# Kernel optimization log

Measured on AMD Instinct MI355X. Metric: run time of the kernel, lower is better.

Reference implementation:

```python
import jax, jax.numpy as jnp
import numpy as np

HS, FF, NH = 1024, 4096, 16
HD = HS // NH
EPS = 1e-5

def _ln(x, g, b):
    m = jnp.mean(x, axis=-1, keepdims=True)
    v = jnp.mean((x - m) ** 2, axis=-1, keepdims=True)
    return (x - m) * jax.lax.rsqrt(v + EPS) * g + b

def setup_inputs() -> dict:
    key = jax.random.key(0)
    ks = jax.random.split(key, 12)
    s = 1.0 / np.sqrt(HS)
    si = 1.0 / np.sqrt(FF)
    d = {
        "hidden_states": jax.random.normal(ks[0], (2, 2048, HS), dtype=jnp.float32),
        "attention_mask": jnp.zeros((2, 1, 1, 2048), dtype=jnp.float32),
        "Wq": jax.random.uniform(ks[1], (HS, HS), minval=-s, maxval=s),
        "bq": jnp.zeros((HS,), jnp.float32),
        "Wk": jax.random.uniform(ks[2], (HS, HS), minval=-s, maxval=s),
        "bk": jnp.zeros((HS,), jnp.float32),
        "Wv": jax.random.uniform(ks[3], (HS, HS), minval=-s, maxval=s),
        "bv": jnp.zeros((HS,), jnp.float32),
        "Wo": jax.random.uniform(ks[4], (HS, HS), minval=-s, maxval=s),
        "bo": jnp.zeros((HS,), jnp.float32),
        "W1": jax.random.uniform(ks[5], (HS, FF), minval=-s, maxval=s),
        "b1": jnp.zeros((FF,), jnp.float32),
        "W2": jax.random.uniform(ks[6], (FF, HS), minval=-si, maxval=si),
        "b2": jnp.zeros((HS,), jnp.float32),
        "ln1_g": jnp.ones((HS,), jnp.float32),
        "ln1_b": jnp.zeros((HS,), jnp.float32),
        "ln2_g": jnp.ones((HS,), jnp.float32),
        "ln2_b": jnp.zeros((HS,), jnp.float32),
    }
    return d

def reference(hidden_states, attention_mask, Wq, bq, Wk, bk, Wv, bv, Wo, bo,
              W1, b1, W2, b2, ln1_g, ln1_b, ln2_g, ln2_b):
    bs, S, _ = hidden_states.shape
    x = hidden_states
    # self-attention (dropout is identity in eval)
    q = (x @ Wq + bq).reshape(bs, S, NH, HD).transpose(0, 2, 1, 3)
    k = (x @ Wk + bk).reshape(bs, S, NH, HD).transpose(0, 2, 1, 3)
    v = (x @ Wv + bv).reshape(bs, S, NH, HD).transpose(0, 2, 1, 3)
    scores = jnp.einsum("bhqd,bhkd->bhqk", q, k) / np.sqrt(HD) + attention_mask
    probs = jax.nn.softmax(scores, axis=-1)
    attn = jnp.einsum("bhqk,bhkd->bhqd", probs, v)
    attn = attn.transpose(0, 2, 1, 3).reshape(bs, S, HS)
    mha = attn @ Wo + bo
    h = _ln(x + mha, ln1_g, ln1_b)
    # FFN
    ff = jax.nn.relu(h @ W1 + b1) @ W2 + b2
    return _ln(h + ff, ln2_g, ln2_b)
```

## Files before the change

kernel.cpp:

```cpp
#include <hip/hip_runtime.h>
#include <hip/hip_bf16.h>

#define HS   1024
#define FF   4096
#define NH   16
#define HD   64
#define SEQ  2048
#define BSZ  2
#define MROWS (BSZ * SEQ)
#define EPS  1e-5f
#define QKV_STRIDE (3 * HS)

typedef float f32x4  __attribute__((ext_vector_type(4)));
typedef short bf16x8 __attribute__((ext_vector_type(8)));

#if __has_builtin(__builtin_amdgcn_exp2f)
#define EXP2(x) __builtin_amdgcn_exp2f(x)
#else
#define EXP2(x) exp2f(x)
#endif

__device__ __forceinline__ unsigned short f2bf(float x) {
  unsigned int u = __float_as_uint(x);
  u += 0x7fffu + ((u >> 16) & 1u);
  return (unsigned short)(u >> 16);
}

__device__ __forceinline__ float bf2f(unsigned short u) {
  return __uint_as_float((unsigned int)u << 16);
}

__device__ __forceinline__ unsigned int pkbf(float a, float b) {
  union { __hip_bfloat162 h; unsigned int u; } x;
  x.h = __float22bfloat162_rn(float2{a, b});
  return x.u;
}

__device__ __forceinline__ void async16(const ushort* g, ushort* lds) {
  __builtin_amdgcn_global_load_lds(
      (const __attribute__((address_space(1))) unsigned int*)g,
      (__attribute__((address_space(3))) unsigned int*)lds, 16, 0, 0);
}

template <int TBM, int TBN, bool RELU, bool OUT_BF16, bool PARTIAL>
__global__ __launch_bounds__(256) void gemm_bf16_kernel(
    const ushort* __restrict__ A, const ushort* __restrict__ Bt,
    const float* __restrict__ bias, void* __restrict__ Cout,
    int M, int N, int K, int kLen, size_t zstride)
{
  constexpr int MI = TBM / 32;
  constexpr int NJ = TBN / 32;
  __shared__ ushort As[TBM * 64];
  __shared__ ushort Bs[TBN * 64];

  const int tid = threadIdx.x;
  const int wv = tid >> 6, ln = tid & 63;

  const unsigned nxy = gridDim.x * gridDim.y;
  unsigned id = blockIdx.y * gridDim.x + blockIdx.x;
  id = (id & 7) * (nxy >> 3) + (id >> 3);
  const int bn = id % gridDim.x, bm = id / gridDim.x;

  const int lr = ln & 15;
  const int lg = ln >> 4;
  const int mrow_base = (wv >> 1) * (TBM / 2);
  const int ncol_base = (wv & 1) * (TBN / 2);

  f32x4 acc[MI][NJ];
#pragma unroll
  for (int i = 0; i < MI; ++i)
#pragma unroll
    for (int j = 0; j < NJ; ++j) acc[i][j] = (f32x4){0.f, 0.f, 0.f, 0.f};

  const int rr = ln >> 3, cc = ln & 7;
  const int kBeg = blockIdx.z * kLen, kEnd = kBeg + kLen;

  for (int k0 = kBeg; k0 < kEnd; k0 += 64) {
    __syncthreads();
#pragma unroll
    for (int t = 0; t < TBM / 32; ++t) {
      const int R = wv * (TBM / 4) + t * 8 + rr;
      const int c = cc ^ (R & 7);
      async16(A + (size_t)(bm * TBM + R) * K + k0 + c * 8,
              &As[(size_t)(wv * (TBM / 4) + t * 8) * 64]);
    }
#pragma unroll
    for (int t = 0; t < TBN / 32; ++t) {
      const int R = wv * (TBN / 4) + t * 8 + rr;
      const int c = cc ^ (R & 7);
      async16(Bt + (size_t)(bn * TBN + R) * K + k0 + c * 8,
              &Bs[(size_t)(wv * (TBN / 4) + t * 8) * 64]);
    }
    __syncthreads();

#pragma unroll
    for (int s = 0; s < 2; ++s) {
      bf16x8 a[MI], b[NJ];
#pragma unroll
      for (int i = 0; i < MI; ++i) {
        const int m = mrow_base + i * 16 + lr;
        a[i] = *(const bf16x8*)&As[(size_t)m * 64 + (((s * 4 + lg) ^ (m & 7)) * 8)];
      }
#pragma unroll
      for (int j = 0; j < NJ; ++j) {
        const int n = ncol_base + j * 16 + lr;
        b[j] = *(const bf16x8*)&Bs[(size_t)n * 64 + (((s * 4 + lg) ^ (n & 7)) * 8)];
      }
#pragma unroll
      for (int i = 0; i < MI; ++i)
#pragma unroll
        for (int j = 0; j < NJ; ++j)
          acc[i][j] = __builtin_amdgcn_mfma_f32_16x16x32_bf16(a[i], b[j], acc[i][j], 0, 0, 0);
    }
  }

  const int gm0 = bm * TBM + mrow_base;
  const int gn0 = bn * TBN + ncol_base;

  if (PARTIAL) {
    float* Cp = (float*)Cout + (size_t)blockIdx.z * zstride;
#pragma unroll
    for (int i = 0; i < MI; ++i)
#pragma unroll
      for (int r = 0; r < 4; ++r) {
        const size_t row = (size_t)(gm0 + i * 16 + lg * 4 + r);
#pragma unroll
        for (int j = 0; j < NJ; ++j)
          Cp[row * N + gn0 + j * 16 + lr] = acc[i][j][r];
      }
  } else {
    float bs4[NJ];
#pragma unroll
    for (int j = 0; j < NJ; ++j) bs4[j] = bias[gn0 + j * 16 + lr];
    float* Cf = (float*)Cout;
    ushort* Cb = (ushort*)Cout;
#pragma unroll
    for (int i = 0; i < MI; ++i) {
#pragma unroll
      for (int r = 0; r < 4; ++r) {
        const size_t row = (size_t)(gm0 + i * 16 + lg * 4 + r);
#pragma unroll
        for (int j = 0; j < NJ; ++j) {
          float val = acc[i][j][r] + bs4[j];
          if (RELU) val = fmaxf(val, 0.f);
          const size_t idx = row * N + gn0 + j * 16 + lr;
          if (OUT_BF16) Cb[idx] = f2bf(val);
          else          Cf[idx] = val;
        }
      }
    }
  }
}

__device__ __forceinline__ void transpose_tile(
    const float* __restrict__ W, ushort* __restrict__ Wt,
    int K, int N, int n0, int k0, int tid, ushort (*T)[72])
{
#pragma unroll
  for (int t = 0; t < 4; ++t) {
    const int r = t * 16 + (tid >> 4);
    const int c = (tid & 15) * 4;
    const float4 w = *(const float4*)&W[(size_t)(k0 + r) * N + n0 + c];
    T[c + 0][r] = f2bf(w.x); T[c + 1][r] = f2bf(w.y);
    T[c + 2][r] = f2bf(w.z); T[c + 3][r] = f2bf(w.w);
  }
  __syncthreads();
#pragma unroll
  for (int t = 0; t < 4; ++t) {
    const int n = t * 16 + (tid >> 4);
    const int kc = (tid & 15) * 4;
    ushort4 o;
    o.x = T[n][kc]; o.y = T[n][kc + 1]; o.z = T[n][kc + 2]; o.w = T[n][kc + 3];
    *(ushort4*)&Wt[(size_t)(n0 + n) * K + k0 + kc] = o;
  }
}

__global__ __launch_bounds__(256) void prep_kernel(
    const float* __restrict__ Wq, const float* __restrict__ Wk,
    const float* __restrict__ Wv, const float* __restrict__ Wo,
    const float* __restrict__ W1, const float* __restrict__ W2,
    const float* __restrict__ bq, const float* __restrict__ bk,
    const float* __restrict__ bv, const float* __restrict__ x,
    const float* __restrict__ mask,
    ushort* __restrict__ Wqkvt, ushort* __restrict__ Wot,
    ushort* __restrict__ W1t, ushort* __restrict__ W2t,
    float* __restrict__ bqkv, ushort* __restrict__ xb,
    float* __restrict__ maskL2)
{
  __shared__ ushort T[64][72];
  const int b = blockIdx.x, tid = threadIdx.x;
  const size_t M1 = 1024 * 1024;
  if (b < 1024) {
    const int w = b >> 8, l = b & 255;
    const int n0 = (l & 15) * 64, k0 = (l >> 4) * 64;
    const float* src = (w == 0) ? Wq : (w == 1) ? Wk : (w == 2) ? Wv : Wo;
    ushort* dst = (w < 3) ? (Wqkvt + (size_t)w * M1) : Wot;
    transpose_tile(src, dst, HS, HS, n0, k0, tid, T);
  } else if (b < 2048) {
    const int l = b - 1024;
    transpose_tile(W1, W1t, HS, FF, (l & 63) * 64, (l >> 6) * 64, tid, T);
  } else if (b < 3072) {
    const int l = b - 2048;
    transpose_tile(W2, W2t, FF, HS, (l & 15) * 64, (l >> 4) * 64, tid, T);
  } else if (b < 5120) {
    const size_t base = (size_t)(b - 3072) * 2048 + tid * 8;
    const float4 v0 = *(const float4*)&x[base];
    const float4 v1 = *(const float4*)&x[base + 4];
    ushort4 o0, o1;
    o0.x = f2bf(v0.x); o0.y = f2bf(v0.y); o0.z = f2bf(v0.z); o0.w = f2bf(v0.w);
    o1.x = f2bf(v1.x); o1.y = f2bf(v1.y); o1.z = f2bf(v1.z); o1.w = f2bf(v1.w);
    *(ushort4*)&xb[base] = o0;
    *(ushort4*)&xb[base + 4] = o1;
  } else {
#pragma unroll
    for (int t = 0; t < 12; ++t) {
      const int i = t * 256 + tid;
      bqkv[i] = (i < HS) ? bq[i] : (i < 2 * HS) ? bk[i - HS] : bv[i - 2 * HS];
    }
#pragma unroll
    for (int t = 0; t < 16; ++t) {
      const int i = t * 256 + tid;
      maskL2[i] = mask[i] * 1.44269504f;
    }
  }
}

__global__ __launch_bounds__(256) void vtrans_kernel(
    const ushort* __restrict__ vb, ushort* __restrict__ VTg, int stride)
{
  __shared__ ushort T[64][68];
  const int tid = threadIdx.x;
  const int s0 = blockIdx.x * 64;
  const int bh = blockIdx.y;
  const int b = bh >> 4, h = bh & 15;
#pragma unroll
  for (int t = 0; t < 4; ++t) {
    const int rr = t * 16 + (tid >> 4);
    const int c4 = (tid & 15) * 4;
    const ushort4 w = *(const ushort4*)&vb[(size_t)(b * SEQ + s0 + rr) * stride + h * 64 + c4];
    T[c4 + 0][rr] = w.x; T[c4 + 1][rr] = w.y;
    T[c4 + 2][rr] = w.z; T[c4 + 3][rr] = w.w;
  }
  __syncthreads();
#pragma unroll
  for (int t = 0; t < 4; ++t) {
    const int d = t * 16 + (tid >> 4);
    const int k4 = (tid & 15) * 4;
    ushort4 o;
    o.x = T[d][k4]; o.y = T[d][k4 + 1]; o.z = T[d][k4 + 2]; o.w = T[d][k4 + 3];
    *(ushort4*)&VTg[((size_t)bh * 64 + d) * SEQ + s0 + k4] = o;
  }
}

__global__ __launch_bounds__(256, 2) void attention_mfma_kernel(
    const ushort* __restrict__ Qb, const ushort* __restrict__ Kb,
    const ushort* __restrict__ VTg, const float* __restrict__ maskL2,
    ushort* __restrict__ O)
{
  __shared__ ushort smem[36864];
  float* mL = (float*)(smem + 32768);

  const int tid = threadIdx.x;
  const int wv = tid >> 6, ln = tid & 63;
  const int c = ln & 15, g = ln >> 4;

  const unsigned d0 = blockIdx.x + 16u * (blockIdx.y + 16u * blockIdx.z);
  const unsigned w0 = (d0 & 7) * 64 + (d0 >> 3);
  const int qt = w0 & 15;
  const int hh = (w0 >> 4) & 15;
  const int b  = w0 >> 8;

  const int bh = b * NH + hh;
  const size_t row0 = (size_t)b * SEQ + (size_t)qt * 128;
  const int ch = hh * HD;
  const int wq0 = wv * 32;

  bf16x8 qf[2][2];
#pragma unroll
  for (int nt = 0; nt < 2; ++nt)
#pragma unroll
    for (int s = 0; s < 2; ++s)
      qf[nt][s] = *(const bf16x8*)&Qb[(row0 + wq0 + nt * 16 + c) * QKV_STRIDE + ch + s * 32 + g * 8];

  const float* mrow = maskL2 + (size_t)b * SEQ;
#pragma unroll
  for (int t = 0; t < 2; ++t)
    async16((const ushort*)(mrow + t * 1024 + wv * 256 + ln * 4),
            (ushort*)(mL + t * 1024 + wv * 256));

  const int rr = ln >> 3, cc = ln & 7;
  const int r4 = ln >> 4, sc = ln & 15;

  auto stage = [&](int kb, int bsel) {
    ushort* Ks  = smem + bsel * 16384;
    ushort* VTs = Ks + 8192;
    const size_t krow0 = (size_t)b * SEQ + (size_t)kb * 128;
#pragma unroll
    for (int t = 0; t < 4; ++t) {
      const int r = wv * 32 + t * 8 + rr;
      async16(Kb + (krow0 + r) * QKV_STRIDE + ch + ((cc ^ (r & 7)) * 8),
              &Ks[(size_t)(wv * 32 + t * 8) * 64]);
    }
#pragma unroll
    for (int t = 0; t < 4; ++t) {
      const int d = wv * 16 + t * 4 + r4;
      const int srcc = (sc & 8) | ((sc & 7) ^ (d & 7));
      async16(VTg + ((size_t)bh * 64 + d) * SEQ + kb * 128 + srcc * 8,
              &VTs[(size_t)(wv * 16 + t * 4) * 128]);
    }
  };

  f32x4 ao[4][2];
#pragma unroll
  for (int i = 0; i < 4; ++i) { ao[i][0] = (f32x4){0,0,0,0}; ao[i][1] = (f32x4){0,0,0,0}; }
  float l_r[2] = {0.f, 0.f};

  stage(0, 0);

  for (int kb = 0; kb < SEQ / 128; ++kb) {
    const int cur = kb & 1;
    __builtin_amdgcn_s_barrier();
    __builtin_amdgcn_sched_barrier(0);
    if (kb + 1 < SEQ / 128) {
      stage(kb + 1, cur ^ 1);
      asm volatile("s_waitcnt vmcnt(8)" ::: "memory");
    } else {
      asm volatile("s_waitcnt vmcnt(0)" ::: "memory");
    }
    __builtin_amdgcn_s_barrier();
    __builtin_amdgcn_sched_barrier(0);

    ushort* Ks  = smem + cur * 16384;
    ushort* VTs = Ks + 8192;

    f32x4 as_[8][2];
#pragma unroll
    for (int i = 0; i < 8; ++i) { as_[i][0] = (f32x4){0,0,0,0}; as_[i][1] = (f32x4){0,0,0,0}; }
    __builtin_amdgcn_s_setprio(1);
#pragma unroll
    for (int s = 0; s < 2; ++s) {
#pragma unroll
      for (int mt = 0; mt < 8; ++mt) {
        const int key = mt * 16 + c;
        const bf16x8 kf = *(const bf16x8*)&Ks[(size_t)key * 64 + (((s * 4 + g) ^ (key & 7)) * 8)];
#pragma unroll
        for (int nt = 0; nt < 2; ++nt)
          as_[mt][nt] = __builtin_amdgcn_mfma_f32_16x16x32_bf16(kf, qf[nt][s], as_[mt][nt], 0, 0, 0);
      }
    }
    __builtin_amdgcn_s_setprio(0);

#pragma unroll
    for (int mt = 0; mt < 8; ++mt) {
      const float4 mk = *(const float4*)&mL[kb * 128 + mt * 16 + g * 4];
      const float mka[4] = {mk.x, mk.y, mk.z, mk.w};
#pragma unroll
      for (int nt = 0; nt < 2; ++nt) {
#pragma unroll
        for (int r = 0; r < 4; ++r) {
          const float p = EXP2(fminf(fmaf(as_[mt][nt][r], 0.18033688f, mka[r]), 86.56f));
          as_[mt][nt][r] = p;
          l_r[nt] += p;
        }
      }
    }

#pragma unroll
    for (int s = 0; s < 4; ++s) {
      bf16x8 pf[2];
#pragma unroll
      for (int nt = 0; nt < 2; ++nt) {
        const unsigned A0 = pkbf(as_[2 * s][nt][0], as_[2 * s][nt][1]);
        const unsigned A1 = pkbf(as_[2 * s][nt][2], as_[2 * s][nt][3]);
        const unsigned B0 = pkbf(as_[2 * s + 1][nt][0], as_[2 * s + 1][nt][1]);
        const unsigned B1 = pkbf(as_[2 * s + 1][nt][2], as_[2 * s + 1][nt][3]);
        auto x0 = __builtin_amdgcn_permlane32_swap(A0, B0, false, false);
        auto x1 = __builtin_amdgcn_permlane32_swap(A1, B1, false, false);
        auto y0 = __builtin_amdgcn_permlane16_swap(x0[0], x0[1], false, false);
        auto y1 = __builtin_amdgcn_permlane16_swap(x1[0], x1[1], false, false);
        union { unsigned w[4]; bf16x8 v; } u;
        u.w[0] = y0[0]; u.w[1] = y1[0]; u.w[2] = y0[1]; u.w[3] = y1[1];
        pf[nt] = u.v;
      }
      __builtin_amdgcn_s_setprio(1);
#pragma unroll
      for (int mt = 0; mt < 4; ++mt) {
        const int d = mt * 16 + c;
        const int k = s * 4 + g;
        const int vslot = (k & 8) | ((k & 7) ^ (d & 7));
        const bf16x8 vf = *(const bf16x8*)&VTs[(size_t)d * 128 + vslot * 8];
#pragma unroll
        for (int nt = 0; nt < 2; ++nt)
          ao[mt][nt] = __builtin_amdgcn_mfma_f32_16x16x32_bf16(vf, pf[nt], ao[mt][nt], 0, 0, 0);
      }
      __builtin_amdgcn_s_setprio(0);
    }
  }

#pragma unroll
  for (int nt = 0; nt < 2; ++nt) {
    l_r[nt] += __shfl_xor(l_r[nt], 16, 64);
    l_r[nt] += __shfl_xor(l_r[nt], 32, 64);
  }

  __syncthreads();
  ushort* OL = smem;
#pragma unroll
  for (int nt = 0; nt < 2; ++nt) {
    const float inv = 1.f / l_r[nt];
    const int q = wq0 + nt * 16 + c;
#pragma unroll
    for (int mt = 0; mt < 4; ++mt) {
      const int d = mt * 16 + g * 4;
      uint2 w;
      w.x = pkbf(ao[mt][nt][0] * inv, ao[mt][nt][1] * inv);
      w.y = pkbf(ao[mt][nt][2] * inv, ao[mt][nt][3] * inv);
      *(uint2*)&OL[q * 72 + d] = w;
    }
  }
  __syncthreads();
#pragma unroll
  for (int it = 0; it < 4; ++it) {
    const int unit = it * 256 + tid;
    const int q = unit >> 3, sg = unit & 7;
    const uint4 w = *(const uint4*)&OL[q * 72 + sg * 8];
    *(uint4*)&O[(row0 + q) * HS + ch + sg * 8] = w;
  }
}

template <bool EMIT16>
__global__ __launch_bounds__(256) void add_ln_red_kernel(
    const float* __restrict__ P0, const float* __restrict__ P1,
    const float* __restrict__ bias, const float* __restrict__ X,
    const float* __restrict__ g, const float* __restrict__ b,
    float* __restrict__ out, ushort* __restrict__ outb)
{
  const int row = blockIdx.x;
  const int tid = threadIdx.x;
  const size_t base = (size_t)row * HS + tid * 4;
  const float4 p0 = *(const float4*)&P0[base];
  const float4 p1 = *(const float4*)&P1[base];
  const float4 bi = *(const float4*)&bias[tid * 4];
  const float4 xv = *(const float4*)&X[base];
  float4 v;
  v.x = xv.x + p0.x + p1.x + bi.x;
  v.y = xv.y + p0.y + p1.y + bi.y;
  v.z = xv.z + p0.z + p1.z + bi.z;
  v.w = xv.w + p0.w + p1.w + bi.w;
  float s1 = v.x + v.y + v.z + v.w;
  float s2 = v.x * v.x + v.y * v.y + v.z * v.z + v.w * v.w;
#pragma unroll
  for (int off = 32; off > 0; off >>= 1) {
    s1 += __shfl_down(s1, off, 64);
    s2 += __shfl_down(s2, off, 64);
  }
  __shared__ float red[8];
  __shared__ float stat[2];
  const int wid = tid >> 6;
  if ((tid & 63) == 0) { red[wid] = s1; red[4 + wid] = s2; }
  __syncthreads();
  if (tid == 0) {
    const float t1 = red[0] + red[1] + red[2] + red[3];
    const float t2 = red[4] + red[5] + red[6] + red[7];
    const float mean = t1 * (1.f / HS);
    const float var = t2 * (1.f / HS) - mean * mean;
    stat[0] = mean;
    stat[1] = rsqrtf(var + EPS);
  }
  __syncthreads();
  const float mean = stat[0], rstd = stat[1];
  const float4 gv = *(const float4*)&g[tid * 4];
  const float4 bv = *(const float4*)&b[tid * 4];
  float4 r;
  r.x = (v.x - mean) * rstd * gv.x + bv.x;
  r.y = (v.y - mean) * rstd * gv.y + bv.y;
  r.z = (v.z - mean) * rstd * gv.z + bv.z;
  r.w = (v.w - mean) * rstd * gv.w + bv.w;
  *(float4*)&out[base] = r;
  if (EMIT16) {
    ushort4 o;
    o.x = f2bf(r.x); o.y = f2bf(r.y); o.z = f2bf(r.z); o.w = f2bf(r.w);
    *(ushort4*)&outb[base] = o;
  }
}

__global__ __launch_bounds__(256) void add_ln_bf16_kernel(
    const ushort* __restrict__ Pb, const float* __restrict__ X,
    const float* __restrict__ g, const float* __restrict__ b,
    float* __restrict__ out, ushort* __restrict__ outb)
{
  const int row = blockIdx.x;
  const int tid = threadIdx.x;
  const size_t base = (size_t)row * HS + tid * 4;
  const ushort4 pb = *(const ushort4*)&Pb[base];
  const float4 xv = *(const float4*)&X[base];
  float4 v;
  v.x = xv.x + bf2f(pb.x);
  v.y = xv.y + bf2f(pb.y);
  v.z = xv.z + bf2f(pb.z);
  v.w = xv.w + bf2f(pb.w);
  float s1 = v.x + v.y + v.z + v.w;
  float s2 = v.x * v.x + v.y * v.y + v.z * v.z + v.w * v.w;
#pragma unroll
  for (int off = 32; off > 0; off >>= 1) {
    s1 += __shfl_down(s1, off, 64);
    s2 += __shfl_down(s2, off, 64);
  }
  __shared__ float red[8];
  __shared__ float stat[2];
  const int wid = tid >> 6;
  if ((tid & 63) == 0) { red[wid] = s1; red[4 + wid] = s2; }
  __syncthreads();
  if (tid == 0) {
    const float t1 = red[0] + red[1] + red[2] + red[3];
    const float t2 = red[4] + red[5] + red[6] + red[7];
    const float mean = t1 * (1.f / HS);
    const float var = t2 * (1.f / HS) - mean * mean;
    stat[0] = mean;
    stat[1] = rsqrtf(var + EPS);
  }
  __syncthreads();
  const float mean = stat[0], rstd = stat[1];
  const float4 gv = *(const float4*)&g[tid * 4];
  const float4 bv = *(const float4*)&b[tid * 4];
  float4 r;
  r.x = (v.x - mean) * rstd * gv.x + bv.x;
  r.y = (v.y - mean) * rstd * gv.y + bv.y;
  r.z = (v.z - mean) * rstd * gv.z + bv.z;
  r.w = (v.w - mean) * rstd * gv.w + bv.w;
  *(float4*)&out[base] = r;
  ushort4 o;
  o.x = f2bf(r.x); o.y = f2bf(r.y); o.z = f2bf(r.z); o.w = f2bf(r.w);
  *(ushort4*)&outb[base] = o;
}

extern "C" void kernel_launch(void* const* d_in, const int* in_sizes, int n_in,
                              void* d_out, int out_size, void* d_ws, size_t ws_size,
                              hipStream_t stream)
{
  const float* x    = (const float*)d_in[0];
  const float* mask = (const float*)d_in[1];
  const float* Wq   = (const float*)d_in[2];  const float* bq  = (const float*)d_in[3];
  const float* Wk   = (const float*)d_in[4];  const float* bk  = (const float*)d_in[5];
  const float* Wv   = (const float*)d_in[6];  const float* bv  = (const float*)d_in[7];
  const float* Wo   = (const float*)d_in[8];  const float* bo  = (const float*)d_in[9];
  const float* W1   = (const float*)d_in[10]; const float* b1  = (const float*)d_in[11];
  const float* W2   = (const float*)d_in[12]; const float* b2  = (const float*)d_in[13];
  const float* g1   = (const float*)d_in[14]; const float* be1 = (const float*)d_in[15];
  const float* g2   = (const float*)d_in[16]; const float* be2 = (const float*)d_in[17];
  float* out = (float*)d_out;

  ushort* wsu = (ushort*)d_ws;
  const size_t M1 = 1024 * 1024;

  ushort* Wqkvt = wsu;
  ushort* Wot   = wsu + 3 * M1;
  ushort* W1t   = wsu + 4 * M1;
  ushort* W2t   = wsu + 8 * M1;
  float*  bqkv  = (float*)(wsu + 12 * M1);
  float*  maskL2= (float*)(wsu + 12 * M1 + 8192);
  ushort* xb    = wsu + 13 * M1;
  ushort* qkvb  = wsu + 17 * M1;
  ushort* VTg   = wsu + 29 * M1;
  ushort* attnb = wsu + 33 * M1;
  ushort* mhab  = wsu + 13 * M1;
  float*  h     = (float*)(wsu + 29 * M1);
  ushort* hb    = wsu + 37 * M1;
  ushort* ff1o  = wsu + 13 * M1;
  float*  ff2P0 = (float*)wsu;
  float*  ff2P1 = (float*)(wsu + 39 * M1);

  const dim3 blk(256);

  prep_kernel<<<dim3(5121), blk, 0, stream>>>(
      Wq, Wk, Wv, Wo, W1, W2, bq, bk, bv, x, mask,
      Wqkvt, Wot, W1t, W2t, bqkv, xb, maskL2);

  gemm_bf16_kernel<128, 128, false, true, false><<<dim3(24, 32), blk, 0, stream>>>(
      xb, Wqkvt, bqkv, qkvb, MROWS, 3 * HS, HS, HS, 0);

  vtrans_kernel<<<dim3(SEQ / 64, BSZ * NH), blk, 0, stream>>>(qkvb + 2 * HS, VTg, QKV_STRIDE);

  attention_mfma_kernel<<<dim3(SEQ / 128, NH, BSZ), blk, 0, stream>>>(
      qkvb, qkvb + HS, VTg, maskL2, attnb);

  gemm_bf16_kernel<64, 128, false, true, false><<<dim3(8, 64), blk, 0, stream>>>(
      attnb, Wot, bo, mhab, MROWS, HS, HS, HS, 0);
  add_ln_bf16_kernel<<<dim3(MROWS), blk, 0, stream>>>(
      mhab, x, g1, be1, h, hb);

  gemm_bf16_kernel<128, 128, true, true, false><<<dim3(32, 32), blk, 0, stream>>>(
      hb, W1t, b1, ff1o, MROWS, FF, HS, HS, 0);
  gemm_bf16_kernel<128, 128, false, false, true><<<dim3(8, 32, 2), blk, 0, stream>>>(
      ff1o, W2t, nullptr, ff2P0, MROWS, HS, FF, FF / 2, (size_t)(ff2P1 - ff2P0));
  add_ln_red_kernel<false><<<dim3(MROWS), blk, 0, stream>>>(
      ff2P0, ff2P1, b2, h, g2, be2, out, nullptr);
}
```

Measured before the change: 368.8 us.

## Halve attention query tile, single-buffer VT, store mask as bf16 for occupancy

The attention kernel now processes 64 queries per block instead of 128 (one 16-row MMA tile per wave), doubling the grid to 1024 blocks. V^T is single-buffered and loaded at the start of each key step, with an extra barrier before PV. The mask is stored in bf16 and the overflow clamp is dropped. These cut shared memory and registers to allow three blocks per CU. The trade-off is that each block reloads K/V for half as many queries, there is one more barrier per iteration, and the mask loses some precision.

```diff
diff --git a/kernel.cpp b/kernel.cpp
--- a/kernel.cpp
+++ b/kernel.cpp
@@ -185,7 +185,7 @@
     ushort* __restrict__ Wqkvt, ushort* __restrict__ Wot,
     ushort* __restrict__ W1t, ushort* __restrict__ W2t,
     float* __restrict__ bqkv, ushort* __restrict__ xb,
-    float* __restrict__ maskL2)
+    ushort* __restrict__ maskL2b)
 {
   __shared__ ushort T[64][72];
   const int b = blockIdx.x, tid = threadIdx.x;
@@ -220,7 +220,7 @@
 #pragma unroll
     for (int t = 0; t < 16; ++t) {
       const int i = t * 256 + tid;
-      maskL2[i] = mask[i] * 1.44269504f;
+      maskL2b[i] = f2bf(mask[i] * 1.44269504f);
     }
   }
 }
@@ -252,48 +252,41 @@
   }
 }
 
-__global__ __launch_bounds__(256, 2) void attention_mfma_kernel(
+__global__ __launch_bounds__(256, 3) void attention_mfma_kernel(
     const ushort* __restrict__ Qb, const ushort* __restrict__ Kb,
-    const ushort* __restrict__ VTg, const float* __restrict__ maskL2,
+    const ushort* __restrict__ VTg, const ushort* __restrict__ maskL2b,
     ushort* __restrict__ O)
 {
-  __shared__ ushort smem[36864];
-  float* mL = (float*)(smem + 32768);
+  __shared__ ushort smem[26624];
+  ushort* mLb = smem + 24576;
 
   const int tid = threadIdx.x;
   const int wv = tid >> 6, ln = tid & 63;
   const int c = ln & 15, g = ln >> 4;
 
-  const unsigned d0 = blockIdx.x + 16u * (blockIdx.y + 16u * blockIdx.z);
-  const unsigned w0 = (d0 & 7) * 64 + (d0 >> 3);
-  const int qt = w0 & 15;
-  const int hh = (w0 >> 4) & 15;
-  const int b  = w0 >> 8;
+  const unsigned d0 = blockIdx.x + 32u * (blockIdx.y + 16u * blockIdx.z);
+  const unsigned w0 = (d0 & 7) * 128 + (d0 >> 3);
+  const int qt = w0 & 31;
+  const int hh = (w0 >> 5) & 15;
+  const int b  = w0 >> 9;
 
   const int bh = b * NH + hh;
-  const size_t row0 = (size_t)b * SEQ + (size_t)qt * 128;
+  const size_t row0 = (size_t)b * SEQ + (size_t)qt * 64;
   const int ch = hh * HD;
-  const int wq0 = wv * 32;
-
-  bf16x8 qf[2][2];
-#pragma unroll
-  for (int nt = 0; nt < 2; ++nt)
-#pragma unroll
-    for (int s = 0; s < 2; ++s)
-      qf[nt][s] = *(const bf16x8*)&Qb[(row0 + wq0 + nt * 16 + c) * QKV_STRIDE + ch + s * 32 + g * 8];
-
-  const float* mrow = maskL2 + (size_t)b * SEQ;
-#pragma unroll
-  for (int t = 0; t < 2; ++t)
-    async16((const ushort*)(mrow + t * 1024 + wv * 256 + ln * 4),
-            (ushort*)(mL + t * 1024 + wv * 256));
+  const int wq0 = wv * 16;
+
+  bf16x8 qf[2];
+#pragma unroll
+  for (int s = 0; s < 2; ++s)
+    qf[s] = *(const bf16x8*)&Qb[(row0 + wq0 + c) * QKV_STRIDE + ch + s * 32 + g * 8];
+
+  async16(&maskL2b[(size_t)b * SEQ + (size_t)(wv * 64 + ln) * 8], &mLb[wv * 512]);
 
   const int rr = ln >> 3, cc = ln & 7;
   const int r4 = ln >> 4, sc = ln & 15;
 
-  auto stage = [&](int kb, int bsel) {
-    ushort* Ks  = smem + bsel * 16384;
-    ushort* VTs = Ks + 8192;
+  auto stageK = [&](int kb, int bsel) {
+    ushort* Ks = smem + bsel * 8192;
     const size_t krow0 = (size_t)b * SEQ + (size_t)kb * 128;
 #pragma unroll
     for (int t = 0; t < 4; ++t) {
@@ -301,6 +294,9 @@
       async16(Kb + (krow0 + r) * QKV_STRIDE + ch + ((cc ^ (r & 7)) * 8),
               &Ks[(size_t)(wv * 32 + t * 8) * 64]);
     }
+  };
+  auto stageVT = [&](int kb) {
+    ushort* VTs = smem + 16384;
 #pragma unroll
     for (int t = 0; t < 4; ++t) {
       const int d = wv * 16 + t * 4 + r4;
@@ -310,32 +306,33 @@
     }
   };
 
-  f32x4 ao[4][2];
-#pragma unroll
-  for (int i = 0; i < 4; ++i) { ao[i][0] = (f32x4){0,0,0,0}; ao[i][1] = (f32x4){0,0,0,0}; }
-  float l_r[2] = {0.f, 0.f};
-
-  stage(0, 0);
+  f32x4 ao[4];
+#pragma unroll
+  for (int i = 0; i < 4; ++i) ao[i] = (f32x4){0.f, 0.f, 0.f, 0.f};
+  float l_r = 0.f;
+
+  stageK(0, 0);
 
   for (int kb = 0; kb < SEQ / 128; ++kb) {
     const int cur = kb & 1;
     __builtin_amdgcn_s_barrier();
     __builtin_amdgcn_sched_barrier(0);
+    stageVT(kb);
     if (kb + 1 < SEQ / 128) {
-      stage(kb + 1, cur ^ 1);
+      stageK(kb + 1, cur ^ 1);
       asm volatile("s_waitcnt vmcnt(8)" ::: "memory");
     } else {
-      asm volatile("s_waitcnt vmcnt(0)" ::: "memory");
+      asm volatile("s_waitcnt vmcnt(4)" ::: "memory");
     }
     __builtin_amdgcn_s_barrier();
     __builtin_amdgcn_sched_barrier(0);
 
-    ushort* Ks  = smem + cur * 16384;
-    ushort* VTs = Ks + 8192;
-
-    f32x4 as_[8][2];
-#pragma unroll
-    for (int i = 0; i < 8; ++i) { as_[i][0] = (f32x4){0,0,0,0}; as_[i][1] = (f32x4){0,0,0,0}; }
+    ushort* Ks  = smem + cur * 8192;
+    ushort* VTs = smem + 16384;
+
+    f32x4 as_[8];
+#pragma unroll
+    for (int i = 0; i < 8; ++i) as_[i] = (f32x4){0.f, 0.f, 0.f, 0.f};
     __builtin_amdgcn_s_setprio(1);
 #pragma unroll
     for (int s = 0; s < 2; ++s) {
@@ -343,45 +340,43 @@
       for (int mt = 0; mt < 8; ++mt) {
         const int key = mt * 16 + c;
         const bf16x8 kf = *(const bf16x8*)&Ks[(size_t)key * 64 + (((s * 4 + g) ^ (key & 7)) * 8)];
-#pragma unroll
-        for (int nt = 0; nt < 2; ++nt)
-          as_[mt][nt] = __builtin_amdgcn_mfma_f32_16x16x32_bf16(kf, qf[nt][s], as_[mt][nt], 0, 0, 0);
+        as_[mt] = __builtin_amdgcn_mfma_f32_16x16x32_bf16(kf, qf[s], as_[mt], 0, 0, 0);
       }
     }
     __builtin_amdgcn_s_setprio(0);
 
 #pragma unroll
     for (int mt = 0; mt < 8; ++mt) {
-      const float4 mk = *(const float4*)&mL[kb * 128 + mt * 16 + g * 4];
-      const float mka[4] = {mk.x, mk.y, mk.z, mk.w};
-#pragma unroll
-      for (int nt = 0; nt < 2; ++nt) {
-#pragma unroll
-        for (int r = 0; r < 4; ++r) {
-          const float p = EXP2(fminf(fmaf(as_[mt][nt][r], 0.18033688f, mka[r]), 86.56f));
-          as_[mt][nt][r] = p;
-          l_r[nt] += p;
-        }
-      }
-    }
+      const ushort4 mu = *(const ushort4*)&mLb[kb * 128 + mt * 16 + g * 4];
+      const float mka[4] = {bf2f(mu.x), bf2f(mu.y), bf2f(mu.z), bf2f(mu.w)};
+#pragma unroll
+      for (int r = 0; r < 4; ++r) {
+        const float p = EXP2(fmaf(as_[mt][r], 0.18033688f, mka[r]));
+        as_[mt][r] = p;
+        l_r += p;
+      }
+    }
+
+    if (kb + 1 < SEQ / 128)
+      asm volatile("s_waitcnt vmcnt(4)" ::: "memory");
+    else
+      asm volatile("s_waitcnt vmcnt(0)" ::: "memory");
+    __builtin_amdgcn_s_barrier();
+    __builtin_amdgcn_sched_barrier(0);
 
 #pragma unroll
     for (int s = 0; s < 4; ++s) {
-      bf16x8 pf[2];
-#pragma unroll
-      for (int nt = 0; nt < 2; ++nt) {
-        const unsigned A0 = pkbf(as_[2 * s][nt][0], as_[2 * s][nt][1]);
-        const unsigned A1 = pkbf(as_[2 * s][nt][2], as_[2 * s][nt][3]);
-        const unsigned B0 = pkbf(as_[2 * s + 1][nt][0], as_[2 * s + 1][nt][1]);
-        const unsigned B1 = pkbf(as_[2 * s + 1][nt][2], as_[2 * s + 1][nt][3]);
-        auto x0 = __builtin_amdgcn_permlane32_swap(A0, B0, false, false);
-        auto x1 = __builtin_amdgcn_permlane32_swap(A1, B1, false, false);
-        auto y0 = __builtin_amdgcn_permlane16_swap(x0[0], x0[1], false, false);
-        auto y1 = __builtin_amdgcn_permlane16_swap(x1[0], x1[1], false, false);
-        union { unsigned w[4]; bf16x8 v; } u;
-        u.w[0] = y0[0]; u.w[1] = y1[0]; u.w[2] = y0[1]; u.w[3] = y1[1];
-        pf[nt] = u.v;
-      }
+      const unsigned A0 = pkbf(as_[2 * s][0], as_[2 * s][1]);
+      const unsigned A1 = pkbf(as_[2 * s][2], as_[2 * s][3]);
+      const unsigned B0 = pkbf(as_[2 * s + 1][0], as_[2 * s + 1][1]);
+      const unsigned B1 = pkbf(as_[2 * s + 1][2], as_[2 * s + 1][3]);
+      auto x0 = __builtin_amdgcn_permlane32_swap(A0, B0, false, false);
+      auto x1 = __builtin_amdgcn_permlane32_swap(A1, B1, false, false);
+      auto y0 = __builtin_amdgcn_permlane16_swap(x0[0], x0[1], false, false);
+      auto y1 = __builtin_amdgcn_permlane16_swap(x1[0], x1[1], false, false);
+      union { unsigned w[4]; bf16x8 v; } u;
+      u.w[0] = y0[0]; u.w[1] = y1[0]; u.w[2] = y0[1]; u.w[3] = y1[1];
+      const bf16x8 pf = u.v;
       __builtin_amdgcn_s_setprio(1);
 #pragma unroll
       for (int mt = 0; mt < 4; ++mt) {
@@ -389,38 +384,32 @@
         const int k = s * 4 + g;
         const int vslot = (k & 8) | ((k & 7) ^ (d & 7));
         const bf16x8 vf = *(const bf16x8*)&VTs[(size_t)d * 128 + vslot * 8];
-#pragma unroll
-        for (int nt = 0; nt < 2; ++nt)
-          ao[mt][nt] = __builtin_amdgcn_mfma_f32_16x16x32_bf16(vf, pf[nt], ao[mt][nt], 0, 0, 0);
+        ao[mt] = __builtin_amdgcn_mfma_f32_16x16x32_bf16(vf, pf, ao[mt], 0, 0, 0);
       }
       __builtin_amdgcn_s_setprio(0);
     }
   }
 
-#pragma unroll
-  for (int nt = 0; nt < 2; ++nt) {
-    l_r[nt] += __shfl_xor(l_r[nt], 16, 64);
-    l_r[nt] += __shfl_xor(l_r[nt], 32, 64);
-  }
+  l_r += __shfl_xor(l_r, 16, 64);
+  l_r += __shfl_xor(l_r, 32, 64);
 
   __syncthreads();
   ushort* OL = smem;
-#pragma unroll
-  for (int nt = 0; nt < 2; ++nt) {
-    const float inv = 1.f / l_r[nt];
-    const int q = wq0 + nt * 16 + c;
+  {
+    const float inv = 1.f / l_r;
+    const int q = wq0 + c;
 #pragma unroll
     for (int mt = 0; mt < 4; ++mt) {
       const int d = mt * 16 + g * 4;
       uint2 w;
-      w.x = pkbf(ao[mt][nt][0] * inv, ao[mt][nt][1] * inv);
-      w.y = pkbf(ao[mt][nt][2] * inv, ao[mt][nt][3] * inv);
+      w.x = pkbf(ao[mt][0] * inv, ao[mt][1] * inv);
+      w.y = pkbf(ao[mt][2] * inv, ao[mt][3] * inv);
       *(uint2*)&OL[q * 72 + d] = w;
     }
   }
   __syncthreads();
 #pragma unroll
-  for (int it = 0; it < 4; ++it) {
+  for (int it = 0; it < 2; ++it) {
     const int unit = it * 256 + tid;
     const int q = unit >> 3, sg = unit & 7;
     const uint4 w = *(const uint4*)&OL[q * 72 + sg * 8];
@@ -558,7 +547,7 @@
   ushort* W1t   = wsu + 4 * M1;
   ushort* W2t   = wsu + 8 * M1;
   float*  bqkv  = (float*)(wsu + 12 * M1);
-  float*  maskL2= (float*)(wsu + 12 * M1 + 8192);
+  ushort* maskL2b = wsu + 12 * M1 + 8192;
   ushort* xb    = wsu + 13 * M1;
   ushort* qkvb  = wsu + 17 * M1;
   ushort* VTg   = wsu + 29 * M1;
@@ -574,15 +563,15 @@
 
   prep_kernel<<<dim3(5121), blk, 0, stream>>>(
       Wq, Wk, Wv, Wo, W1, W2, bq, bk, bv, x, mask,
-      Wqkvt, Wot, W1t, W2t, bqkv, xb, maskL2);
+      Wqkvt, Wot, W1t, W2t, bqkv, xb, maskL2b);
 
   gemm_bf16_kernel<128, 128, false, true, false><<<dim3(24, 32), blk, 0, stream>>>(
       xb, Wqkvt, bqkv, qkvb, MROWS, 3 * HS, HS, HS, 0);
 
   vtrans_kernel<<<dim3(SEQ / 64, BSZ * NH), blk, 0, stream>>>(qkvb + 2 * HS, VTg, QKV_STRIDE);
 
-  attention_mfma_kernel<<<dim3(SEQ / 128, NH, BSZ), blk, 0, stream>>>(
-      qkvb, qkvb + HS, VTg, maskL2, attnb);
+  attention_mfma_kernel<<<dim3(SEQ / 64, NH, BSZ), blk, 0, stream>>>(
+      qkvb, qkvb + HS, VTg, maskL2b, attnb);
 
   gemm_bf16_kernel<64, 128, false, true, false><<<dim3(8, 64), blk, 0, stream>>>(
       attnb, Wot, bo, mhab, MROWS, HS, HS, HS, 0);
```

New measurement: 374.1 us. No clear change (+1.4%).
